# Performance work log

Hardware: AMD Instinct MI355X
Metric: run time of the kernel (lower is better)

## Reference

```python
import jax, jax.numpy as jnp
import numpy as np

PLOGIT_INIT = 1.5

def setup_inputs() -> dict:
    key = jax.random.key(0)
    B, C, H, W = 32, 256, 64, 64
    x = jax.random.normal(key, (B, C, H, W), dtype=jnp.float32)
    plogit = jnp.full((C,), PLOGIT_INIT, dtype=jnp.float32)  # learned param (post channel-expansion)
    return {"input": x, "plogit": plogit}


def reference(input, plogit):
    B, C = input.shape[0], input.shape[1]
    x = input.reshape(B * C, -1)                       # [B*C, HW]  (to_cw)
    s = jnp.sort(x, axis=-1)                           # per-row full sort
    N = s.shape[1]
    p = jax.nn.sigmoid(plogit)                         # [C]
    # torch: p.view(1,-1).repeat(B,1).view(-1) -> channel-major tiling over batch
    p_full = jnp.tile(p, B)                            # [B*C]
    # torch indexes with int(N * p.data[0] -/+ 0.02): a single scalar column index
    p0 = jax.lax.stop_gradient(p[0])
    i_low = jnp.clip((N * (p0 - 0.02)).astype(jnp.int32), 0, N - 1)
    i_high = jnp.clip((N * (p0 + 0.02)).astype(jnp.int32), 0, N - 1)
    x_low = jax.lax.stop_gradient(jnp.take(s, i_low, axis=1))    # [B*C], detached
    x_high = jax.lax.stop_gradient(jnp.take(s, i_high, axis=1))  # [B*C], detached
    thr = x_low + (x_high - x_low) * p_full            # linear interp, grad flows via p
    thr = thr.reshape(B, C, 1, 1)                      # from_cw
    return jax.nn.relu(input - thr)
```

## Files before the change

kernel.cpp:

```cpp
#include <hip/hip_runtime.h>
#include <math.h>

#define NTHREADS 256
#define NELEM    4096
#define EPL      64
#define NREP     8
#define HSTRIDE  260
#define WHSIZE   (NREP * HSTRIDE)

__device__ __forceinline__ unsigned f2ord(float f) {
    unsigned u = __float_as_uint(f);
    return (u & 0x80000000u) ? ~u : (u | 0x80000000u);
}
__device__ __forceinline__ float ord2f(unsigned k) {
    unsigned u = (k & 0x80000000u) ? (k ^ 0x80000000u) : ~k;
    return __uint_as_float(u);
}

__device__ __forceinline__ void zero_region(unsigned* h, int lane, int nuint4) {
    uint4* p = (uint4*)h;
    for (int i = lane; i < nuint4; i += 64) p[i] = make_uint4(0u, 0u, 0u, 0u);
}

template <int NR>
__device__ __forceinline__ void hist_pass(const unsigned* k, unsigned* h, int lane,
                                          unsigned known, unsigned pref, int shift) {
    unsigned* my = h + ((NR > 1) ? (lane & (NR - 1)) * HSTRIDE : 0);
    #pragma unroll
    for (int j = 0; j < EPL; ++j) {
        unsigned kk = k[j];
        if ((kk & known) == pref)
            atomicAdd(&my[(kk >> shift) & 0xFFu], 1u);
    }
}

struct Pick2 { unsigned a, b; };

template <int NR>
__device__ __forceinline__ Pick2 wave_pick2(const unsigned* region, int lane,
                                            unsigned rA, unsigned rB) {
    unsigned s0 = 0, s1 = 0, s2 = 0, s3 = 0;
    #pragma unroll
    for (int rep = 0; rep < NR; ++rep) {
        uint4 h = ((const uint4*)(region + rep * HSTRIDE))[lane];
        s0 += h.x; s1 += h.y; s2 += h.z; s3 += h.w;
    }
    unsigned lp1 = s0, lp2 = s0 + s1, lp3 = s0 + s1 + s2, tot = lp3 + s3;
    unsigned scan = tot;
    #pragma unroll
    for (int off = 1; off < 64; off <<= 1) {
        unsigned v = __shfl_up(scan, off, 64);
        if (lane >= off) scan += v;
    }
    unsigned ex = scan - tot;
    unsigned base[4] = {ex, ex + lp1, ex + lp2, ex + lp3};
    unsigned cnt[4]  = {s0, s1, s2, s3};
    unsigned resA = 0, resB = 0;
    bool fA = false, fB = false;
    #pragma unroll
    for (int j = 0; j < 4; ++j) {
        if (rA >= base[j] && rA < base[j] + cnt[j]) {
            resA = ((unsigned)(4 * lane + j) << 12) | (rA - base[j]); fA = true;
        }
        if (rB >= base[j] && rB < base[j] + cnt[j]) {
            resB = ((unsigned)(4 * lane + j) << 12) | (rB - base[j]); fB = true;
        }
    }
    unsigned long long mA = __ballot(fA);
    unsigned long long mB = __ballot(fB);
    Pick2 r;
    r.a = __shfl(resA, (int)(__ffsll((long long)mA) - 1), 64);
    r.b = __shfl(resB, (int)(__ffsll((long long)mB) - 1), 64);
    return r;
}

__global__ void __launch_bounds__(NTHREADS, 4)
xsrelu_kernel(const float* __restrict__ x, const float* __restrict__ plogit,
              float* __restrict__ out, int C) {
    __shared__ __align__(16) unsigned hist[4][WHSIZE];

    const int wave = threadIdx.x >> 6;
    const int lane = threadIdx.x & 63;
    const int row  = blockIdx.x * 4 + wave;

    const float4* xr = (const float4*)(x + (size_t)row * NELEM);
    unsigned k[EPL];
    #pragma unroll
    for (int j = 0; j < EPL / 4; ++j) {
        float4 v = xr[j * 64 + lane];
        k[4 * j + 0] = f2ord(v.x);
        k[4 * j + 1] = f2ord(v.y);
        k[4 * j + 2] = f2ord(v.z);
        k[4 * j + 3] = f2ord(v.w);
    }

    float p0 = 1.0f / (1.0f + expf(-plogit[0]));
    float pc = 1.0f / (1.0f + expf(-plogit[row % C]));
    int kLow  = min(max((int)((float)NELEM * (p0 - 0.02f)), 0), NELEM - 1);
    int kHigh = min(max((int)((float)NELEM * (p0 + 0.02f)), 0), NELEM - 1);

    unsigned* hw = hist[wave];
    unsigned prefA = 0u, prefB = 0u, known = 0u;
    unsigned rA = (unsigned)kLow, rB = (unsigned)kHigh;
    int shift;
    bool diverged = false;

    #pragma unroll 1
    for (shift = 24; shift >= 0; shift -= 8) {
        if (diverged) break;
        zero_region(hw, lane, WHSIZE / 4);
        __threadfence_block();
        hist_pass<NREP>(k, hw, lane, known, prefA, shift);
        __threadfence_block();
        Pick2 p = wave_pick2<NREP>(hw, lane, rA, rB);
        unsigned bA = p.a >> 12, bB = p.b >> 12;
        prefA |= bA << shift;  rA = p.a & 0xFFFu;
        prefB |= bB << shift;  rB = p.b & 0xFFFu;
        known |= 0xFFu << shift;
        diverged = (bA != bB);
        __threadfence_block();
    }

    unsigned knownA = known, knownB = known;
    #pragma unroll 1
    for (int s = shift; s >= 0; s -= 8) {
        zero_region(hw, lane, (HSTRIDE + 3) / 4);
        __threadfence_block();
        hist_pass<1>(k, hw, lane, knownA, prefA, s);
        __threadfence_block();
        Pick2 p = wave_pick2<1>(hw, lane, rA, rA);
        prefA |= (p.a >> 12) << s;
        rA = p.a & 0xFFFu;
        knownA |= 0xFFu << s;
        __threadfence_block();
    }
    #pragma unroll 1
    for (int s = shift; s >= 0; s -= 8) {
        zero_region(hw, lane, (HSTRIDE + 3) / 4);
        __threadfence_block();
        hist_pass<1>(k, hw, lane, knownB, prefB, s);
        __threadfence_block();
        Pick2 p = wave_pick2<1>(hw, lane, rB, rB);
        prefB |= (p.a >> 12) << s;
        rB = p.a & 0xFFFu;
        knownB |= 0xFFu << s;
        __threadfence_block();
    }

    float xlow  = ord2f(prefA);
    float xhigh = ord2f(prefB);
    float thr = xlow + (xhigh - xlow) * pc;

    float4* outr = (float4*)(out + (size_t)row * NELEM);
    #pragma unroll
    for (int j = 0; j < EPL / 4; ++j) {
        float4 o;
        o.x = fmaxf(ord2f(k[4 * j + 0]) - thr, 0.0f);
        o.y = fmaxf(ord2f(k[4 * j + 1]) - thr, 0.0f);
        o.z = fmaxf(ord2f(k[4 * j + 2]) - thr, 0.0f);
        o.w = fmaxf(ord2f(k[4 * j + 3]) - thr, 0.0f);
        outr[j * 64 + lane] = o;
    }
}

extern "C" void kernel_launch(void* const* d_in, const int* in_sizes, int n_in,
                              void* d_out, int out_size, void* d_ws, size_t ws_size,
                              hipStream_t stream) {
    const float* x      = (const float*)d_in[0];
    const float* plogit = (const float*)d_in[1];
    float* out          = (float*)d_out;
    int C    = in_sizes[1];
    int rows = in_sizes[0] / NELEM;
    xsrelu_kernel<<<rows / 4, NTHREADS, 0, stream>>>(x, plogit, out, C);
}
```

Baseline: 271.7 us.

## Split each row across two waves and merge divergent radix-select passes

Each row is now handled by two waves (128 threads) instead of one, halving the per-thread element registers from 64 to 32 and launching twice as many blocks. After the two target ranks diverge, the separate sequential refinement loops for the low and high thresholds are merged into the main loop, with a second small histogram region for the high rank. The change trades wave-local fences for block-wide __syncthreads and shares histogram atomics across waves, aiming at better occupancy and fewer serial passes. Removing the occupancy hint from the launch bounds also changes register allocation.

```diff
diff --git a/kernel.cpp b/kernel.cpp
--- a/kernel.cpp
+++ b/kernel.cpp
@@ -3,10 +3,13 @@
 
 #define NTHREADS 256
 #define NELEM    4096
-#define EPL      64
-#define NREP     8
+#define EPL      32
+#define NREPA    8
+#define NREPB    2
 #define HSTRIDE  260
-#define WHSIZE   (NREP * HSTRIDE)
+#define ASIZE    (NREPA * HSTRIDE)
+#define BSIZE    (NREPB * HSTRIDE)
+#define ROWLDS   (ASIZE + BSIZE)
 
 __device__ __forceinline__ unsigned f2ord(float f) {
     unsigned u = __float_as_uint(f);
@@ -15,23 +18,6 @@
 __device__ __forceinline__ float ord2f(unsigned k) {
     unsigned u = (k & 0x80000000u) ? (k ^ 0x80000000u) : ~k;
     return __uint_as_float(u);
-}
-
-__device__ __forceinline__ void zero_region(unsigned* h, int lane, int nuint4) {
-    uint4* p = (uint4*)h;
-    for (int i = lane; i < nuint4; i += 64) p[i] = make_uint4(0u, 0u, 0u, 0u);
-}
-
-template <int NR>
-__device__ __forceinline__ void hist_pass(const unsigned* k, unsigned* h, int lane,
-                                          unsigned known, unsigned pref, int shift) {
-    unsigned* my = h + ((NR > 1) ? (lane & (NR - 1)) * HSTRIDE : 0);
-    #pragma unroll
-    for (int j = 0; j < EPL; ++j) {
-        unsigned kk = k[j];
-        if ((kk & known) == pref)
-            atomicAdd(&my[(kk >> shift) & 0xFFu], 1u);
-    }
 }
 
 struct Pick2 { unsigned a, b; };
@@ -74,20 +60,23 @@
     return r;
 }
 
-__global__ void __launch_bounds__(NTHREADS, 4)
+__global__ void __launch_bounds__(NTHREADS)
 xsrelu_kernel(const float* __restrict__ x, const float* __restrict__ plogit,
               float* __restrict__ out, int C) {
-    __shared__ __align__(16) unsigned hist[4][WHSIZE];
+    __shared__ __align__(16) unsigned hist[2][ROWLDS];
 
-    const int wave = threadIdx.x >> 6;
-    const int lane = threadIdx.x & 63;
-    const int row  = blockIdx.x * 4 + wave;
+    const int wid   = threadIdx.x >> 6;
+    const int lane  = threadIdx.x & 63;
+    const int rhalf = wid & 1;
+    const int rloc  = wid >> 1;
+    const int row   = blockIdx.x * 2 + rloc;
+    const int rlane = rhalf * 64 + lane;
 
     const float4* xr = (const float4*)(x + (size_t)row * NELEM);
     unsigned k[EPL];
     #pragma unroll
     for (int j = 0; j < EPL / 4; ++j) {
-        float4 v = xr[j * 64 + lane];
+        float4 v = xr[j * 128 + rlane];
         k[4 * j + 0] = f2ord(v.x);
         k[4 * j + 1] = f2ord(v.y);
         k[4 * j + 2] = f2ord(v.z);
@@ -99,52 +88,49 @@
     int kLow  = min(max((int)((float)NELEM * (p0 - 0.02f)), 0), NELEM - 1);
     int kHigh = min(max((int)((float)NELEM * (p0 + 0.02f)), 0), NELEM - 1);
 
-    unsigned* hw = hist[wave];
+    unsigned* hA  = hist[rloc];
+    unsigned* hB  = hA + ASIZE;
+    unsigned* myA = hA + (rhalf * 4 + (lane & 3)) * HSTRIDE;
+    unsigned* myB = hB + rhalf * HSTRIDE;
+
     unsigned prefA = 0u, prefB = 0u, known = 0u;
     unsigned rA = (unsigned)kLow, rB = (unsigned)kHigh;
-    int shift;
     bool diverged = false;
 
     #pragma unroll 1
-    for (shift = 24; shift >= 0; shift -= 8) {
-        if (diverged) break;
-        zero_region(hw, lane, WHSIZE / 4);
-        __threadfence_block();
-        hist_pass<NREP>(k, hw, lane, known, prefA, shift);
-        __threadfence_block();
-        Pick2 p = wave_pick2<NREP>(hw, lane, rA, rB);
-        unsigned bA = p.a >> 12, bB = p.b >> 12;
-        prefA |= bA << shift;  rA = p.a & 0xFFFu;
-        prefB |= bB << shift;  rB = p.b & 0xFFFu;
+    for (int shift = 24; shift >= 0; shift -= 8) {
+        uint4* hz = (uint4*)hA;
+        #pragma unroll 1
+        for (int i = rlane; i < ROWLDS / 4; i += 128)
+            hz[i] = make_uint4(0u, 0u, 0u, 0u);
+        __syncthreads();
+
+        #pragma unroll
+        for (int j = 0; j < EPL; ++j) {
+            unsigned kk = k[j];
+            if ((kk & known) == prefA)
+                atomicAdd(&myA[(kk >> shift) & 0xFFu], 1u);
+        }
+        if (diverged) {
+            #pragma unroll
+            for (int j = 0; j < EPL; ++j) {
+                unsigned kk = k[j];
+                if ((kk & known) == prefB)
+                    atomicAdd(&myB[(kk >> shift) & 0xFFu], 1u);
+            }
+        }
+        __syncthreads();
+
+        Pick2 p = wave_pick2<NREPA>(hA, lane, rA, diverged ? rA : rB);
+        unsigned pA = p.a, pB = p.b;
+        if (diverged)
+            pB = wave_pick2<NREPB>(hB, lane, rB, rB).a;
+        unsigned bA = pA >> 12, bB = pB >> 12;
+        prefA |= bA << shift;  rA = pA & 0xFFFu;
+        prefB |= bB << shift;  rB = pB & 0xFFFu;
+        diverged = diverged || (bA != bB);
         known |= 0xFFu << shift;
-        diverged = (bA != bB);
-        __threadfence_block();
-    }
-
-    unsigned knownA = known, knownB = known;
-    #pragma unroll 1
-    for (int s = shift; s >= 0; s -= 8) {
-        zero_region(hw, lane, (HSTRIDE + 3) / 4);
-        __threadfence_block();
-        hist_pass<1>(k, hw, lane, knownA, prefA, s);
-        __threadfence_block();
-        Pick2 p = wave_pick2<1>(hw, lane, rA, rA);
-        prefA |= (p.a >> 12) << s;
-        rA = p.a & 0xFFFu;
-        knownA |= 0xFFu << s;
-        __threadfence_block();
-    }
-    #pragma unroll 1
-    for (int s = shift; s >= 0; s -= 8) {
-        zero_region(hw, lane, (HSTRIDE + 3) / 4);
-        __threadfence_block();
-        hist_pass<1>(k, hw, lane, knownB, prefB, s);
-        __threadfence_block();
-        Pick2 p = wave_pick2<1>(hw, lane, rB, rB);
-        prefB |= (p.a >> 12) << s;
-        rB = p.a & 0xFFFu;
-        knownB |= 0xFFu << s;
-        __threadfence_block();
+        __syncthreads();
     }
 
     float xlow  = ord2f(prefA);
@@ -159,7 +145,7 @@
         o.y = fmaxf(ord2f(k[4 * j + 1]) - thr, 0.0f);
         o.z = fmaxf(ord2f(k[4 * j + 2]) - thr, 0.0f);
         o.w = fmaxf(ord2f(k[4 * j + 3]) - thr, 0.0f);
-        outr[j * 64 + lane] = o;
+        outr[j * 128 + rlane] = o;
     }
 }
 
@@ -171,5 +157,5 @@
     float* out          = (float*)d_out;
     int C    = in_sizes[1];
     int rows = in_sizes[0] / NELEM;
-    xsrelu_kernel<<<rows / 4, NTHREADS, 0, stream>>>(x, plogit, out, C);
+    xsrelu_kernel<<<rows / 2, NTHREADS, 0, stream>>>(x, plogit, out, C);
 }
```

After: 239.0 us. -12.0%, faster.
